# Optimization experiments

Measured on AMD Instinct MI355X. Metric: run time of the kernel, lower is better.

## Reference

```python
import jax, jax.numpy as jnp
import numpy as np

N, D, G = 16384, 2048, 4096  # points, vocab_size (feature dim), num_groups


def setup_inputs() -> dict:
    key = jax.random.key(0)
    kx, ke = jax.random.split(key)
    x = jax.random.normal(kx, (N, D), dtype=jnp.float32)
    # trunc_normal_ init for the codebook; plain normal is fine for a numeric reference
    emb = jax.random.truncated_normal(ke, -2.0, 2.0, (G, D), dtype=jnp.float32)
    return {"x": x, "emb": emb}


def reference(x, emb):
    x2 = jnp.sum(x * x, axis=-1, keepdims=True)          # [N, 1]
    e2 = jnp.sum(emb * emb, axis=-1)                     # [G]
    sq = x2 + e2[None, :] - 2.0 * (x @ emb.T)            # [N, G]
    dist = jnp.sqrt(jnp.maximum(sq, 0.0))
    return -dist
```

## Files before the change

kernel.cpp:

```cpp
#include <hip/hip_runtime.h>
#include <hip/hip_bf16.h>

#define NPTS 16384
#define DIM  2048
#define NGRP 4096
#define BKF  128
#define NTF  (DIM / BKF)

typedef __bf16 bf16x8 __attribute__((ext_vector_type(8)));
typedef unsigned short u16x8 __attribute__((ext_vector_type(8)));
typedef float f32x4 __attribute__((ext_vector_type(4)));
typedef int i32x4 __attribute__((ext_vector_type(4)));
typedef int i32x8 __attribute__((ext_vector_type(8)));

__device__ __forceinline__ unsigned short f2bf(float f) {
  union { float f; unsigned u; } v; v.f = f;
  unsigned u = v.u;
  return (unsigned short)((u + 0x7FFFu + ((u >> 16) & 1u)) >> 16);
}
__device__ __forceinline__ float bflo(unsigned u) { return __uint_as_float(u << 16); }
__device__ __forceinline__ float bfhi(unsigned u) { return __uint_as_float(u & 0xffff0000u); }

__device__ __forceinline__ unsigned cvtpk4(float a, float b, float c, float d) {
  int w = __builtin_amdgcn_cvt_pk_fp8_f32(a, b, 0, false);
  w = __builtin_amdgcn_cvt_pk_fp8_f32(c, d, w, true);
  return (unsigned)w;
}

__device__ __forceinline__ void gload16(const void* g, void* lds) {
  __builtin_amdgcn_global_load_lds(
      (const __attribute__((address_space(1))) unsigned*)g,
      (__attribute__((address_space(3))) unsigned*)lds, 16, 0, 0);
}

__device__ __forceinline__ bool sniff_bf16(const void* X) {
  const int lane = threadIdx.x & 63;
  unsigned hb = (((const unsigned short*)X)[lane] >> 8) & 0x7Fu;
  unsigned long long m = __ballot(hb >= 0x3Bu && hb <= 0x41u);
  return __popcll(m) >= 48;
}

__global__ __launch_bounds__(256) void prep_all_kernel(
    const void* __restrict__ Xin, const void* __restrict__ Ein,
    unsigned char* __restrict__ Xf8, unsigned char* __restrict__ Ef8,
    float* __restrict__ x2, float* __restrict__ e2) {
  const int lane  = threadIdx.x & 63;
  const int wavei = threadIdx.x >> 6;
  const bool isbf = sniff_bf16(Xin);

  const int grow = blockIdx.x * 4 + wavei;
  const void* in; unsigned char* q; float* nrm; int row;
  if (grow < NPTS) { in = Xin; q = Xf8; nrm = x2; row = grow; }
  else             { in = Ein; q = Ef8; nrm = e2; row = grow - NPTS; }

  unsigned char* qq = q + (size_t)row * DIM;
  float s = 0.f;
#pragma unroll
  for (int it = 0; it < 4; ++it) {
    float v0, v1, v2, v3, v4, v5, v6, v7;
    if (isbf) {
      const unsigned short* p = (const unsigned short*)in + (size_t)row * DIM;
      uint4 r = *(const uint4*)(p + it * 512 + lane * 8);
      v0 = bflo(r.x); v1 = bfhi(r.x); v2 = bflo(r.y); v3 = bfhi(r.y);
      v4 = bflo(r.z); v5 = bfhi(r.z); v6 = bflo(r.w); v7 = bfhi(r.w);
    } else {
      const float* p = (const float*)in + (size_t)row * DIM;
      float4 a = *(const float4*)(p + it * 512 + lane * 8);
      float4 b = *(const float4*)(p + it * 512 + lane * 8 + 4);
      v0 = a.x; v1 = a.y; v2 = a.z; v3 = a.w;
      v4 = b.x; v5 = b.y; v6 = b.z; v7 = b.w;
    }
    s += v0 * v0 + v1 * v1 + v2 * v2 + v3 * v3;
    s += v4 * v4 + v5 * v5 + v6 * v6 + v7 * v7;
    uint2 w;
    w.x = cvtpk4(v0, v1, v2, v3);
    w.y = cvtpk4(v4, v5, v6, v7);
    *(uint2*)(qq + it * 512 + lane * 8) = w;
  }
#pragma unroll
  for (int off = 32; off > 0; off >>= 1) s += __shfl_down(s, off, 64);
  if (lane == 0) nrm[row] = s;
}

__global__ __launch_bounds__(512, 2) void gemm_mx_kernel(
    const void* __restrict__ Xin,
    const unsigned char* __restrict__ X8, const unsigned char* __restrict__ E8,
    const float* __restrict__ x2, const float* __restrict__ e2,
    void* __restrict__ outv) {
  __shared__ __align__(16) unsigned char sbuf[2][65536];

  const int tid  = threadIdx.x;
  const int lane = tid & 63;
  const int wave = tid >> 6;
  const int wm   = wave >> 2;
  const int wn   = wave & 3;
  const int quad = lane >> 4;
  const int l16  = lane & 15;

  const bool isbf = sniff_bf16(Xin);

  const int rowBase = blockIdx.y * 256;
  const int colBase = blockIdx.x * 256;

  const int srow  = tid >> 3;
  const int scol  = ((tid & 7) ^ (srow & 7)) * 16;
  size_t gAo[4], gBo[4];
#pragma unroll
  for (int g = 0; g < 4; ++g) {
    gAo[g] = (size_t)(rowBase + g * 64 + srow) * DIM + scol;
    gBo[g] = (size_t)(colBase + g * 64 + srow) * DIM + scol;
  }

  const int cb0 = ((quad * 2) ^ (l16 & 7)) * 16;

  f32x4 acc[8][4];
#pragma unroll
  for (int mt = 0; mt < 8; ++mt)
#pragma unroll
    for (int nt = 0; nt < 4; ++nt) acc[mt][nt] = f32x4{0.f, 0.f, 0.f, 0.f};

  i32x8 a8[4], b8[4];

#define STAGE(t_) do { unsigned char* sb_ = sbuf[(t_) & 1];                     \
    const size_t kk_ = (size_t)(t_) * BKF;                                      \
    _Pragma("unroll") for (int g = 0; g < 4; ++g)                               \
      gload16(X8 + gAo[g] + kk_, sb_ + g * 8192 + wave * 1024);                 \
    _Pragma("unroll") for (int g = 0; g < 4; ++g)                               \
      gload16(E8 + gBo[g] + kk_, sb_ + 32768 + g * 8192 + wave * 1024);         \
  } while (0)

#define LDFRAG(dst_, base_, rowi_) do {                                         \
    const unsigned char* p_ = (base_) + (rowi_) * 128;                          \
    i32x4 lo_ = *(const i32x4*)(const void*)(p_ + cb0);                         \
    i32x4 hi_ = *(const i32x4*)(const void*)(p_ + (cb0 ^ 16));                  \
    dst_[0] = lo_[0]; dst_[1] = lo_[1]; dst_[2] = lo_[2]; dst_[3] = lo_[3];     \
    dst_[4] = hi_[0]; dst_[5] = hi_[1]; dst_[6] = hi_[2]; dst_[7] = hi_[3];     \
  } while (0)

#define MFMA16(MOFF_) do {                                                      \
    __builtin_amdgcn_s_setprio(1);                                              \
    _Pragma("unroll") for (int m = 0; m < 4; ++m)                               \
      _Pragma("unroll") for (int n = 0; n < 4; ++n)                             \
        acc[(MOFF_) + m][n] = __builtin_amdgcn_mfma_scale_f32_16x16x128_f8f6f4( \
            a8[m], b8[n], acc[(MOFF_) + m][n], 0, 0,                            \
            0, 0x7F7F7F7F, 0, 0x7F7F7F7F);           \
    __builtin_amdgcn_s_setprio(0);                                              \
  } while (0)

#define BODY(t_, DOSTAGE_, VMS_) do {                                           \
    asm volatile("s_waitcnt vmcnt(" VMS_ ")" ::: "memory");                     \
    __builtin_amdgcn_s_barrier();                                               \
    __builtin_amdgcn_sched_barrier(0);                                          \
    const unsigned char* sa_ = sbuf[(t_) & 1];                                  \
    const unsigned char* sb2_ = sa_ + 32768;                                    \
    _Pragma("unroll") for (int m = 0; m < 4; ++m)                               \
      LDFRAG(a8[m], sa_, (wm * 128 + m * 16 + l16));                            \
    _Pragma("unroll") for (int n = 0; n < 4; ++n)                               \
      LDFRAG(b8[n], sb2_, (wn * 64 + n * 16 + l16));                            \
    MFMA16(0);                                                                  \
    _Pragma("unroll") for (int m = 0; m < 4; ++m)                               \
      LDFRAG(a8[m], sa_, (wm * 128 + (m + 4) * 16 + l16));                      \
    MFMA16(4);                                                                  \
    asm volatile("" ::: "memory");                                              \
    __builtin_amdgcn_s_barrier();                                               \
    __builtin_amdgcn_sched_barrier(0);                                          \
    if (DOSTAGE_) STAGE((t_) + 2);                                              \
  } while (0)

  STAGE(0); STAGE(1);

#pragma unroll 1
  for (int t = 0; t < NTF - 2; ++t) {
    BODY(t, true, "8");
  }
  BODY(NTF - 2, false, "8");
  BODY(NTF - 1, false, "0");
#undef BODY
#undef MFMA16
#undef LDFRAG
#undef STAGE

  float ec[4];
#pragma unroll
  for (int nt = 0; nt < 4; ++nt) ec[nt] = e2[colBase + wn * 64 + nt * 16 + l16];

  if (isbf) {
    unsigned short* out = (unsigned short*)outv;
#pragma unroll
    for (int mt = 0; mt < 8; ++mt)
#pragma unroll
      for (int r2 = 0; r2 < 4; ++r2) {
        const int row = rowBase + wm * 128 + mt * 16 + quad * 4 + r2;
        const float xr = x2[row];
#pragma unroll
        for (int nt = 0; nt < 4; ++nt) {
          const int col = colBase + wn * 64 + nt * 16 + l16;
          float sq = xr + ec[nt] - 2.0f * acc[mt][nt][r2];
          sq = sq > 0.f ? sq : 0.f;
          out[(size_t)row * NGRP + col] = f2bf(-__builtin_sqrtf(sq));
        }
      }
  } else {
    float* out = (float*)outv;
#pragma unroll
    for (int mt = 0; mt < 8; ++mt)
#pragma unroll
      for (int r2 = 0; r2 < 4; ++r2) {
        const int row = rowBase + wm * 128 + mt * 16 + quad * 4 + r2;
        const float xr = x2[row];
#pragma unroll
        for (int nt = 0; nt < 4; ++nt) {
          const int col = colBase + wn * 64 + nt * 16 + l16;
          float sq = xr + ec[nt] - 2.0f * acc[mt][nt][r2];
          sq = sq > 0.f ? sq : 0.f;
          out[(size_t)row * NGRP + col] = -__builtin_sqrtf(sq);
        }
      }
  }
}


__global__ void sniff_kernel(const unsigned short* __restrict__ X, int* __restrict__ flag) {
  if (threadIdx.x == 0 && blockIdx.x == 0) {
    int c = 0;
    for (int i = 0; i < 64; ++i) {
      unsigned b = (X[i] >> 8) & 0x7F;
      c += (b >= 0x3B && b <= 0x41) ? 1 : 0;
    }
    *flag = (c >= 48) ? 1 : 0;
  }
}

__global__ __launch_bounds__(256) void rownorm_kernel(const void* __restrict__ in,
                                                      float* __restrict__ out,
                                                      const int* __restrict__ flag) {
  const int wave = threadIdx.x >> 6;
  const int lane = threadIdx.x & 63;
  const int row  = blockIdx.x * 4 + wave;
  float s = 0.f;
  if (*flag) {
    const unsigned short* p = (const unsigned short*)in + (size_t)row * DIM;
#pragma unroll
    for (int it = 0; it < 4; ++it) {
      uint4 v = *(const uint4*)(p + it * 512 + lane * 8);
      float f;
      f = bflo(v.x); s += f * f;  f = bfhi(v.x); s += f * f;
      f = bflo(v.y); s += f * f;  f = bfhi(v.y); s += f * f;
      f = bflo(v.z); s += f * f;  f = bfhi(v.z); s += f * f;
      f = bflo(v.w); s += f * f;  f = bfhi(v.w); s += f * f;
    }
  } else {
    const float* p = (const float*)in + (size_t)row * DIM;
#pragma unroll
    for (int it = 0; it < 4; ++it) {
      float4 a = *(const float4*)(p + it * 512 + lane * 8);
      float4 b = *(const float4*)(p + it * 512 + lane * 8 + 4);
      s += a.x * a.x + a.y * a.y + a.z * a.z + a.w * a.w;
      s += b.x * b.x + b.y * b.y + b.z * b.z + b.w * b.w;
    }
  }
#pragma unroll
  for (int off = 32; off > 0; off >>= 1) s += __shfl_down(s, off, 64);
  if (lane == 0) out[row] = s;
}

__device__ __forceinline__ u16x8 cvt8(const float* p) {
  float4 a = *(const float4*)p;
  float4 b = *(const float4*)(p + 4);
  u16x8 r;
  r[0] = f2bf(a.x); r[1] = f2bf(a.y); r[2] = f2bf(a.z); r[3] = f2bf(a.w);
  r[4] = f2bf(b.x); r[5] = f2bf(b.y); r[6] = f2bf(b.z); r[7] = f2bf(b.w);
  return r;
}

__global__ __launch_bounds__(256) void gemm_dist_kernel(
    const void* __restrict__ Xv, const void* __restrict__ Ev,
    const float* __restrict__ x2, const float* __restrict__ e2,
    void* __restrict__ outv, const int* __restrict__ flag) {
  __shared__ __align__(16) unsigned short sA[128 * 32];
  __shared__ __align__(16) unsigned short sB[128 * 32];

  const bool isbf = (*flag != 0);
  const int tid  = threadIdx.x;
  const int lane = tid & 63;
  const int wave = tid >> 6;
  const int wm   = wave >> 1;
  const int wn   = wave & 1;
  const int quad = lane >> 4;
  const int l16  = lane & 15;

  const int rowBase = blockIdx.y * 128;
  const int colBase = blockIdx.x * 128;

  const int flat0 = tid * 8;
  const int flat1 = (tid + 256) * 8;
  const int r0 = flat0 >> 5, c0 = flat0 & 31;
  const int r1 = flat1 >> 5, c1 = flat1 & 31;

  const size_t iA0 = (size_t)(rowBase + r0) * DIM + c0;
  const size_t iA1 = (size_t)(rowBase + r1) * DIM + c1;
  const size_t iB0 = (size_t)(colBase + r0) * DIM + c0;
  const size_t iB1 = (size_t)(colBase + r1) * DIM + c1;

  f32x4 zero = {0.f, 0.f, 0.f, 0.f};
  f32x4 acc[4][4];
#pragma unroll
  for (int mt = 0; mt < 4; ++mt)
#pragma unroll
    for (int nt = 0; nt < 4; ++nt) acc[mt][nt] = zero;

  for (int k0 = 0; k0 < DIM; k0 += 32) {
    if (isbf) {
      const unsigned short* X = (const unsigned short*)Xv;
      const unsigned short* E = (const unsigned short*)Ev;
      *(uint4*)(sA + flat0) = *(const uint4*)(X + iA0 + k0);
      *(uint4*)(sA + flat1) = *(const uint4*)(X + iA1 + k0);
      *(uint4*)(sB + flat0) = *(const uint4*)(E + iB0 + k0);
      *(uint4*)(sB + flat1) = *(const uint4*)(E + iB1 + k0);
    } else {
      const float* X = (const float*)Xv;
      const float* E = (const float*)Ev;
      *(u16x8*)(sA + flat0) = cvt8(X + iA0 + k0);
      *(u16x8*)(sA + flat1) = cvt8(X + iA1 + k0);
      *(u16x8*)(sB + flat0) = cvt8(E + iB0 + k0);
      *(u16x8*)(sB + flat1) = cvt8(E + iB1 + k0);
    }
    __syncthreads();

    bf16x8 a[4], b[4];
#pragma unroll
    for (int mt = 0; mt < 4; ++mt)
      a[mt] = *(const bf16x8*)(const void*)(sA + (wm * 64 + mt * 16 + l16) * 32 + quad * 8);
#pragma unroll
    for (int nt = 0; nt < 4; ++nt)
      b[nt] = *(const bf16x8*)(const void*)(sB + (wn * 64 + nt * 16 + l16) * 32 + quad * 8);
#pragma unroll
    for (int mt = 0; mt < 4; ++mt)
#pragma unroll
      for (int nt = 0; nt < 4; ++nt)
        acc[mt][nt] = __builtin_amdgcn_mfma_f32_16x16x32_bf16(a[mt], b[nt], acc[mt][nt], 0, 0, 0);
    __syncthreads();
  }

  float ec[4];
#pragma unroll
  for (int nt = 0; nt < 4; ++nt) ec[nt] = e2[colBase + wn * 64 + nt * 16 + l16];

  if (isbf) {
    unsigned short* out = (unsigned short*)outv;
#pragma unroll
    for (int mt = 0; mt < 4; ++mt)
#pragma unroll
      for (int r = 0; r < 4; ++r) {
        const int row = rowBase + wm * 64 + mt * 16 + quad * 4 + r;
        const float xr = x2[row];
#pragma unroll
        for (int nt = 0; nt < 4; ++nt) {
          const int col = colBase + wn * 64 + nt * 16 + l16;
          float sq = xr + ec[nt] - 2.0f * acc[mt][nt][r];
          sq = sq > 0.f ? sq : 0.f;
          out[(size_t)row * NGRP + col] = f2bf(-__builtin_sqrtf(sq));
        }
      }
  } else {
    float* out = (float*)outv;
#pragma unroll
    for (int mt = 0; mt < 4; ++mt)
#pragma unroll
      for (int r = 0; r < 4; ++r) {
        const int row = rowBase + wm * 64 + mt * 16 + quad * 4 + r;
        const float xr = x2[row];
#pragma unroll
        for (int nt = 0; nt < 4; ++nt) {
          const int col = colBase + wn * 64 + nt * 16 + l16;
          float sq = xr + ec[nt] - 2.0f * acc[mt][nt][r];
          sq = sq > 0.f ? sq : 0.f;
          out[(size_t)row * NGRP + col] = -__builtin_sqrtf(sq);
        }
      }
  }
}

extern "C" void kernel_launch(void* const* d_in, const int* in_sizes, int n_in,
                              void* d_out, int out_size, void* d_ws, size_t ws_size,
                              hipStream_t stream) {
  const size_t xf8 = (size_t)NPTS * DIM;
  const size_t ef8 = (size_t)NGRP * DIM;
  const size_t need = xf8 + ef8 + (NPTS + NGRP) * sizeof(float) + 64;

  if (ws_size >= need) {
    unsigned char* Xf8 = (unsigned char*)d_ws;
    unsigned char* Ef8 = Xf8 + xf8;
    float* x2 = (float*)(Ef8 + ef8);
    float* e2 = x2 + NPTS;

    prep_all_kernel<<<(NPTS + NGRP) / 4, 256, 0, stream>>>(d_in[0], d_in[1],
                                                           Xf8, Ef8, x2, e2);
    dim3 grid(NGRP / 256, NPTS / 256);
    gemm_mx_kernel<<<grid, 512, 0, stream>>>(d_in[0], Xf8, Ef8, x2, e2, d_out);
  } else {
    float* x2 = (float*)d_ws;
    float* e2 = x2 + NPTS;
    int* flag = (int*)(e2 + NGRP);

    sniff_kernel<<<1, 64, 0, stream>>>((const unsigned short*)d_in[0], flag);
    rownorm_kernel<<<NPTS / 4, 256, 0, stream>>>(d_in[0], x2, flag);
    rownorm_kernel<<<NGRP / 4, 256, 0, stream>>>(d_in[1], e2, flag);
    dim3 grid(NGRP / 128, NPTS / 128);
    gemm_dist_kernel<<<grid, 256, 0, stream>>>(d_in[0], d_in[1], x2, e2, d_out, flag);
  }
}
```

Before: 508.2 us.

## Replace double-buffered LDS pipeline with single buffer to fit two blocks per CU

```diff
diff --git a/kernel.cpp b/kernel.cpp
--- a/kernel.cpp
+++ b/kernel.cpp
@@ -87,7 +87,7 @@
     const unsigned char* __restrict__ X8, const unsigned char* __restrict__ E8,
     const float* __restrict__ x2, const float* __restrict__ e2,
     void* __restrict__ outv) {
-  __shared__ __align__(16) unsigned char sbuf[2][65536];
+  __shared__ __align__(16) unsigned char sbuf[65536];
 
   const int tid  = threadIdx.x;
   const int lane = tid & 63;
@@ -121,12 +121,12 @@
 
   i32x8 a8[4], b8[4];
 
-#define STAGE(t_) do { unsigned char* sb_ = sbuf[(t_) & 1];                     \
+#define STAGE(t_) do {                                                          \
     const size_t kk_ = (size_t)(t_) * BKF;                                      \
     _Pragma("unroll") for (int g = 0; g < 4; ++g)                               \
-      gload16(X8 + gAo[g] + kk_, sb_ + g * 8192 + wave * 1024);                 \
+      gload16(X8 + gAo[g] + kk_, sbuf + g * 8192 + wave * 1024);                \
     _Pragma("unroll") for (int g = 0; g < 4; ++g)                               \
-      gload16(E8 + gBo[g] + kk_, sb_ + 32768 + g * 8192 + wave * 1024);         \
+      gload16(E8 + gBo[g] + kk_, sbuf + 32768 + g * 8192 + wave * 1024);        \
   } while (0)
 
 #define LDFRAG(dst_, base_, rowi_) do {                                         \
@@ -147,35 +147,29 @@
     __builtin_amdgcn_s_setprio(0);                                              \
   } while (0)
 
-#define BODY(t_, DOSTAGE_, VMS_) do {                                           \
-    asm volatile("s_waitcnt vmcnt(" VMS_ ")" ::: "memory");                     \
-    __builtin_amdgcn_s_barrier();                                               \
-    __builtin_amdgcn_sched_barrier(0);                                          \
-    const unsigned char* sa_ = sbuf[(t_) & 1];                                  \
-    const unsigned char* sb2_ = sa_ + 32768;                                    \
-    _Pragma("unroll") for (int m = 0; m < 4; ++m)                               \
-      LDFRAG(a8[m], sa_, (wm * 128 + m * 16 + l16));                            \
-    _Pragma("unroll") for (int n = 0; n < 4; ++n)                               \
-      LDFRAG(b8[n], sb2_, (wn * 64 + n * 16 + l16));                            \
-    MFMA16(0);                                                                  \
-    _Pragma("unroll") for (int m = 0; m < 4; ++m)                               \
-      LDFRAG(a8[m], sa_, (wm * 128 + (m + 4) * 16 + l16));                      \
-    MFMA16(4);                                                                  \
-    asm volatile("" ::: "memory");                                              \
-    __builtin_amdgcn_s_barrier();                                               \
-    __builtin_amdgcn_sched_barrier(0);                                          \
-    if (DOSTAGE_) STAGE((t_) + 2);                                              \
-  } while (0)
-
-  STAGE(0); STAGE(1);
-
 #pragma unroll 1
-  for (int t = 0; t < NTF - 2; ++t) {
-    BODY(t, true, "8");
-  }
-  BODY(NTF - 2, false, "8");
-  BODY(NTF - 1, false, "0");
-#undef BODY
+  for (int t = 0; t < NTF; ++t) {
+    __builtin_amdgcn_s_barrier();
+    __builtin_amdgcn_sched_barrier(0);
+    STAGE(t);
+    asm volatile("s_waitcnt vmcnt(0)" ::: "memory");
+    __builtin_amdgcn_s_barrier();
+    __builtin_amdgcn_sched_barrier(0);
+    const unsigned char* sa_ = sbuf;
+    const unsigned char* sb2_ = sbuf + 32768;
+#pragma unroll
+    for (int m = 0; m < 4; ++m)
+      LDFRAG(a8[m], sa_, (wm * 128 + m * 16 + l16));
+#pragma unroll
+    for (int n = 0; n < 4; ++n)
+      LDFRAG(b8[n], sb2_, (wn * 64 + n * 16 + l16));
+    MFMA16(0);
+#pragma unroll
+    for (int m = 0; m < 4; ++m)
+      LDFRAG(a8[m], sa_, (wm * 128 + (m + 4) * 16 + l16));
+    MFMA16(4);
+    asm volatile("" ::: "memory");
+  }
 #undef MFMA16
 #undef LDFRAG
 #undef STAGE
```

Measured after the change: 536.5 us. +5.6%, slower.
